# Optimization experiments

Measured on AMD Instinct MI355X. Metric: run time of the kernel, lower is better.

Reference implementation:

```python
import jax, jax.numpy as jnp
import numpy as np

UNITS, LATENT = 512, 128
CMD = max(int(0.4 * (UNITS - LATENT)), 1)   # 153 command neurons (AutoNCP rule)
INTER = (UNITS - LATENT) - CMD              # 231 inter neurons
SIZES = [INTER, CMD, LATENT]                # hidden size of each wiring layer
INS = [1, INTER, CMD]                       # input size of each wiring layer
B, T = 512, 512
SPARSITY = 0.5                              # AutoNCP default sparsity level


def _linear_init(key, out_dim, in_dim):
    k1, k2 = jax.random.split(key)
    lim = 1.0 / np.sqrt(in_dim)
    W = jax.random.uniform(k1, (out_dim, in_dim), minval=-lim, maxval=lim, dtype=jnp.float32)
    b = jax.random.uniform(k2, (out_dim,), minval=-lim, maxval=lim, dtype=jnp.float32)
    return W, b


def setup_inputs() -> dict:
    key = jax.random.key(0)
    ks = jax.random.split(key, 20)
    inp = {
        'elapsed_times': jax.random.uniform(ks[0], (B, T, 1), dtype=jnp.float32),
        'encoder_hidden': jax.random.normal(ks[1], (B, UNITS), dtype=jnp.float32),
    }
    ki = 2
    for l in range(3):
        cat = INS[l] + SIZES[l]
        for name in ('ff1', 'ff2', 'ta', 'tb'):
            W, bvec = _linear_init(ks[ki], SIZES[l], cat); ki += 1
            inp[f'W_{name}_{l}'] = W
            inp[f'b_{name}_{l}'] = bvec
        m = jax.random.bernoulli(ks[ki], 1.0 - SPARSITY, (INS[l], SIZES[l])).astype(jnp.float32); ki += 1
        # WiredCfCCell: recurrent block of the sparsity mask is all-ones; mask is [h, in+h]
        inp[f'mask_{l}'] = jnp.concatenate([m, jnp.ones((SIZES[l], SIZES[l]), jnp.float32)], axis=0).T
    return inp


def _cfc_cell(x_in, h, W1, b1, W2, b2, Wa, ba, Wb, bb, mask):
    x = jnp.concatenate([x_in, h], axis=-1)          # [B, in+h]
    ff1 = jnp.tanh(x @ (W1 * mask).T + b1)
    ff2 = jnp.tanh(x @ (W2 * mask).T + b2)
    # ts = 1.0 (CfC default when no timespans tensor is passed)
    t_interp = jax.nn.sigmoid((x @ Wa.T + ba) + (x @ Wb.T + bb))
    return ff1 * (1.0 - t_interp) + t_interp * ff2


def _forward(elapsed_times, encoder_hidden, layers):
    h0 = encoder_hidden[:, :INTER]
    h1 = encoder_hidden[:, INTER:INTER + CMD]
    h2 = encoder_hidden[:, INTER + CMD:]

    def step(carry, x_t):
        c0, c1, c2 = carry
        n0 = _cfc_cell(x_t, c0, *layers[0])
        n1 = _cfc_cell(n0, c1, *layers[1])
        n2 = _cfc_cell(n1, c2, *layers[2])
        return (n0, n1, n2), n2

    xs = jnp.swapaxes(elapsed_times, 0, 1)           # [T, B, 1]
    (h0, h1, h2), outs = jax.lax.scan(step, (h0, h1, h2), xs)
    rnn_out = jnp.swapaxes(outs, 0, 1)               # [B, T, LATENT]
    rnn_hidden = jnp.concatenate([h0, h1, h2], axis=1)  # [B, UNITS]
    return rnn_out, rnn_hidden


def reference(elapsed_times, encoder_hidden,
              W_ff1_0, b_ff1_0, W_ff2_0, b_ff2_0, W_ta_0, b_ta_0, W_tb_0, b_tb_0, mask_0,
              W_ff1_1, b_ff1_1, W_ff2_1, b_ff2_1, W_ta_1, b_ta_1, W_tb_1, b_tb_1, mask_1,
              W_ff1_2, b_ff1_2, W_ff2_2, b_ff2_2, W_ta_2, b_ta_2, W_tb_2, b_tb_2, mask_2):
    layers = [
        (W_ff1_0, b_ff1_0, W_ff2_0, b_ff2_0, W_ta_0, b_ta_0, W_tb_0, b_tb_0, mask_0),
        (W_ff1_1, b_ff1_1, W_ff2_1, b_ff2_1, W_ta_1, b_ta_1, W_tb_1, b_tb_1, mask_1),
        (W_ff1_2, b_ff1_2, W_ff2_2, b_ff2_2, W_ta_2, b_ta_2, W_tb_2, b_tb_2, mask_2),
    ]
    return _forward(elapsed_times, encoder_hidden, layers)
```

## Files before the change

### kernel.cpp

```cpp
#include <hip/hip_runtime.h>
#include <stdint.h>

#define B_ 512
#define T_ 512

typedef __attribute__((ext_vector_type(8))) __bf16 bf16x8;
typedef __attribute__((ext_vector_type(4))) float f32x4;
typedef __attribute__((ext_vector_type(8))) unsigned short u16x8;

#define N0OFF 1916928u
#define N1OFF 3194880u
#define N2OFF 4046848u
#define FLOFF 4767744u

constexpr int L_[9]   = {0,0,0, 1,1,1,1, 2,2};
constexpr int NT0_[9] = {0,5,10, 0,3,6,8, 0,4};
constexpr int NT_[9]  = {5,5,5, 3,3,2,2, 4,4};
constexpr int KT_[3]  = {8,12,9};
constexpr int NPT_[3] = {15,10,8};
constexpr int SC_[3]  = {231,153,128};
constexpr int RS_[3]  = {264,392,296};
constexpr int CB_[3]  = {0,231,384};
constexpr unsigned WOFF_[3] = {0u,184320u,368640u};
constexpr int RGO_[9] = {0,27,54, 0,16,32,43, 0,22};
constexpr int RGC_[9] = {27,27,24, 16,16,11,9, 22,22};
constexpr int RGV_[9] = {80,80,71, 48,48,32,25, 64,64};
constexpr int RGB_[9] = {0,80,160, 0,48,96,128, 0,64};
constexpr int RCH4_[3] = {312,208,176};
constexpr int WN_[9] = {6,6,6, 5,5,5,5, 1,1};
constexpr int WF_[9][6] = {
  {1,2,3,4,5,6},{0,2,3,4,5,6},{0,1,3,4,5,6},
  {4,5,6,7,8,0},{3,5,6,7,8,0},{3,4,6,7,8,0},{3,4,5,7,8,0},
  {8,0,0,0,0,0},{7,0,0,0,0,0}};
constexpr int WL_[9][6] = {
  {-1,-1,-2,-2,-2,-2},{-1,-1,-2,-2,-2,-2},{-1,-1,-2,-2,-2,-2},
  {-1,-1,-1,-2,-2,0},{-1,-1,-1,-2,-2,0},{-1,-1,-1,-2,-2,0},{-1,-1,-1,-2,-2,0},
  {-1,0,0,0,0,0},{-1,0,0,0,0,0}};

static __device__ __forceinline__ uint16_t bfbits(float f){
  __bf16 h = (__bf16)f; return __builtin_bit_cast(uint16_t, h);
}
static __device__ __forceinline__ float sigm_f(float x){
  return __builtin_amdgcn_rcpf(1.0f + __builtin_amdgcn_exp2f(-1.4426950408889634f*x));
}
static __device__ __forceinline__ float tanh_f(float x){
  return 2.0f*__builtin_amdgcn_rcpf(1.0f + __builtin_amdgcn_exp2f(-2.8853900817779268f*x)) - 1.0f;
}
static __device__ __forceinline__ uint64_t ldg64(const uint16_t* p){
  return __hip_atomic_load((const unsigned long long*)p, __ATOMIC_RELAXED,
                           __HIP_MEMORY_SCOPE_AGENT);
}
static __device__ __forceinline__ void stg64(uint16_t* p, uint64_t v){
  __hip_atomic_store((unsigned long long*)p, v, __ATOMIC_RELAXED,
                     __HIP_MEMORY_SCOPE_AGENT);
}
#define BAR() do { asm volatile("s_waitcnt lgkmcnt(0)" ::: "memory"); \
                   __builtin_amdgcn_s_barrier(); } while(0)
#define DRAIN() asm volatile("s_waitcnt vmcnt(0)" ::: "memory")

__global__ void zero_flags(uint8_t* wsb){
  int i = blockIdx.x*512 + threadIdx.x;
  if (i < 2304) ((int*)(wsb + FLOFF))[i] = 0;
}

__global__ void pack_w(const float* __restrict__ W1, const float* __restrict__ W2,
                       const float* __restrict__ Wa, const float* __restrict__ Wb,
                       const float* __restrict__ Msk, uint16_t* __restrict__ dst,
                       int NPT, int KT, int S, int C)
{
  int c = blockIdx.x * 256 + threadIdx.x;
  int chunks = 3 * NPT * KT * 64;
  if (c >= chunks) return;
  int perN = KT * 64;
  int n3 = c / perN, r = c % perN;
  int kt = r >> 6, lane = r & 63;
  int m = n3 / NPT, nt = n3 % NPT;
  int j = nt * 16 + (lane & 15);
  int kb = kt * 32 + (lane >> 4) * 8;
  u16x8 o;
  #pragma unroll
  for (int i = 0; i < 8; ++i){
    int k = kb + i;
    float v = 0.f;
    if (j < S && k < C){
      size_t idx = (size_t)j * C + k;
      if (m == 0)      v = W1[idx] * Msk[idx];
      else if (m == 1) v = W2[idx] * Msk[idx];
      else             v = Wa[idx] + Wb[idx];
    }
    o[i] = bfbits(v);
  }
  *(u16x8*)(dst + (size_t)c * 8) = o;
}

template<int SID>
__device__ __forceinline__ void stage_run(
    int g, int tid,
    const float* __restrict__ elapsed, const float* __restrict__ enc,
    const float* __restrict__ bp1, const float* __restrict__ bp2,
    const float* __restrict__ bpa, const float* __restrict__ bpb,
    const uint16_t* __restrict__ Wp, uint8_t* __restrict__ wsb,
    float* __restrict__ out, uint16_t* Wl, uint16_t* XA, uint16_t* HST)
{
  constexpr int LAYER = L_[SID];
  constexpr int NT0 = NT0_[SID], NT = NT_[SID];
  constexpr int KT = KT_[LAYER], NPT = NPT_[LAYER];
  constexpr int SCOL = SC_[LAYER], RS = RS_[LAYER];
  constexpr int CBASE = CB_[LAYER];
  constexpr int NCH = RGC_[SID], RGO = RGO_[SID], RGV = RGV_[SID], RGB = RGB_[SID];
  constexpr int RCH4 = RCH4_[LAYER];

  const int wave = tid >> 6, lane = tid & 63, llo = lane & 15, lhi = lane >> 4;
  const int rowg = tid >> 4, cg = tid & 15;
  const int b0 = g * 32;

  uint16_t* R0 = (uint16_t*)(wsb + N0OFF) + (size_t)g * 39936;
  uint16_t* R1 = (uint16_t*)(wsb + N1OFF) + (size_t)g * 26624;
  uint16_t* R2 = (uint16_t*)(wsb + N2OFF) + (size_t)g * 22528;
  int* FLG = (int*)(wsb + FLOFF) + g * (9*16);
  uint16_t* RNG = (LAYER==0) ? R0 : (LAYER==1) ? R1 : R2;

  {
    const u16x8* Wp8 = (const u16x8*)(Wp + WOFF_[LAYER]);
    u16x8* Wl8 = (u16x8*)Wl;
    constexpr int CHUNKS = 3 * NT * KT * 64;
    for (int c = tid; c < CHUNKS; c += 512){
      int m = c / (NT*KT*64), r = c - m*(NT*KT*64);
      int tl = r / (KT*64),  r2 = r - tl*(KT*64);
      Wl8[c] = Wp8[(size_t)((m*NPT + NT0 + tl)*KT*64) + r2];
    }
  }
  for (int i = tid; i < 32*RS; i += 512) XA[i] = 0;

  float bs0 = 0.f, bs1 = 0.f, bs2 = 0.f;
  if (wave < NT){
    const int j = (NT0 + wave)*16 + llo;
    if (j < SCOL){ bs0 = bp1[j]; bs1 = bp2[j]; bs2 = bpa[j] + bpb[j]; }
  }

  auto chunk_store = [&](int slot, uint16_t tag){
    for (int idx = tid; idx < 32*NCH; idx += 512){
      int row = idx / NCH, c = idx - row*NCH;
      int lc = 3*c;
      uint16_t p0 = (lc+0 < RGV) ? HST[row*80 + lc+0] : (uint16_t)0;
      uint16_t p1 = (lc+1 < RGV) ? HST[row*80 + lc+1] : (uint16_t)0;
      uint16_t p2 = (lc+2 < RGV) ? HST[row*80 + lc+2] : (uint16_t)0;
      uint64_t v = (uint64_t)p0 | ((uint64_t)p1<<16) | ((uint64_t)p2<<32)
                 | ((uint64_t)tag<<48);
      stg64(RNG + (size_t)(slot*32 + row)*RCH4 + (size_t)(RGO + c)*4, v);
    }
  };

  for (int idx = tid; idx < 32*NT*16; idx += 512){
    int row = idx / (NT*16), lc = idx % (NT*16);
    int j = RGB + lc;
    float v = (j < SCOL) ? enc[(size_t)(b0+row)*512 + CBASE + j] : 0.f;
    HST[row*80 + lc] = bfbits(v);
  }
  __syncthreads();
  chunk_store(3, 0xFFFFu);
  DRAIN();
  __syncthreads();
  if (tid == 0)
    __hip_atomic_store(&FLG[SID*16], 1, __ATOMIC_RELAXED, __HIP_MEMORY_SCOPE_AGENT);

  const size_t OH = (size_t)B_ * T_ * 128;

  int fc[6];
  #pragma unroll
  for (int i = 0; i < 6; ++i) fc[i] = 1;

  #pragma unroll 1
  for (int t = 0; t < T_; ++t){
    if (tid == 0){
      bool need = false;
      #pragma unroll
      for (int i = 0; i < WN_[SID]; ++i) need |= (fc[i] < t + WL_[SID][i]);
      if (need){
        int spin = 0;
        for (;;){
          bool ok = true;
          #pragma unroll
          for (int i = 0; i < WN_[SID]; ++i){
            if (fc[i] < t + WL_[SID][i])
              fc[i] = __hip_atomic_load(&FLG[WF_[SID][i]*16], __ATOMIC_RELAXED,
                                        __HIP_MEMORY_SCOPE_AGENT);
            ok &= (fc[i] >= t + WL_[SID][i]);
          }
          if (ok) break;
          __builtin_amdgcn_s_sleep(1);
          if ((++spin & 63) == 0)
            (void)__hip_atomic_load(&FLG[WF_[SID][0]*16], __ATOMIC_ACQUIRE,
                                    __HIP_MEMORY_SCOPE_AGENT);
        }
      }
    }
    BAR();

    {
      uint16_t* drow = XA + rowg * RS;
      constexpr int DST0 = (LAYER==0) ? 1 : (LAYER==1) ? 231 : 153;
      for (int lc = cg; lc < RGV; lc += 16)
        drow[DST0 + RGB + lc] = HST[rowg*80 + lc];

      const uint16_t eN = (uint16_t)t, eH = (uint16_t)(t-1);
      if constexpr (LAYER == 0){
        const uint16_t* rb = R0 + (size_t)((((t+3)&3)*32) + rowg) * 312;
        constexpr int OLO = RGO, OHI = RGO + NCH;
        uint64_t v[5]; uint32_t pend = 0;
        #pragma unroll
        for (int i = 0; i < 5; ++i){
          int c = cg + 16*i;
          if (c < 78 && !(c >= OLO && c < OHI)) pend |= 1u<<i;
        }
        while (pend){
          #pragma unroll
          for (int i = 0; i < 5; ++i)
            if (pend & (1u<<i)) v[i] = ldg64(rb + 4*(cg + 16*i));
          uint32_t np = 0;
          #pragma unroll
          for (int i = 0; i < 5; ++i)
            if ((pend & (1u<<i)) && (uint16_t)(v[i]>>48) != eH) np |= 1u<<i;
          pend = np;
          if (pend) __builtin_amdgcn_s_sleep(1);
        }
        #pragma unroll
        for (int i = 0; i < 5; ++i){
          int c = cg + 16*i;
          if (c >= 78 || (c >= OLO && c < OHI)) continue;
          int rgb, rgv, cr;
          if (c < 27){ rgb=0; rgv=80; cr=c; }
          else if (c < 54){ rgb=80; rgv=80; cr=c-27; }
          else { rgb=160; rgv=71; cr=c-54; }
          int base = 3*cr;
          if (base+0 < rgv) drow[1 + rgb + base+0] = (uint16_t)(v[i]);
          if (base+1 < rgv) drow[1 + rgb + base+1] = (uint16_t)(v[i]>>16);
          if (base+2 < rgv) drow[1 + rgb + base+2] = (uint16_t)(v[i]>>32);
        }
        if (cg == 0) drow[0] = bfbits(elapsed[(size_t)(b0 + rowg)*T_ + t]);
      } else if constexpr (LAYER == 1){
        const uint16_t* rbA = R0 + (size_t)(((t&3)*32) + rowg) * 312;
        const uint16_t* rbB = R1 + (size_t)((((t+3)&3)*32) + rowg) * 208;
        constexpr int OLO = RGO, OHI = RGO + NCH;
        uint64_t vA[5], vB[4]; uint32_t pend = 0;
        #pragma unroll
        for (int i = 0; i < 5; ++i){ int c = cg + 16*i; if (c < 78) pend |= 1u<<i; }
        #pragma unroll
        for (int i = 0; i < 4; ++i){
          int c = cg + 16*i;
          if (c < 52 && !(c >= OLO && c < OHI)) pend |= 1u<<(8+i);
        }
        while (pend){
          #pragma unroll
          for (int i = 0; i < 5; ++i)
            if (pend & (1u<<i)) vA[i] = ldg64(rbA + 4*(cg + 16*i));
          #pragma unroll
          for (int i = 0; i < 4; ++i)
            if (pend & (1u<<(8+i))) vB[i] = ldg64(rbB + 4*(cg + 16*i));
          uint32_t np = 0;
          #pragma unroll
          for (int i = 0; i < 5; ++i)
            if ((pend & (1u<<i)) && (uint16_t)(vA[i]>>48) != eN) np |= 1u<<i;
          #pragma unroll
          for (int i = 0; i < 4; ++i)
            if ((pend & (1u<<(8+i))) && (uint16_t)(vB[i]>>48) != eH) np |= 1u<<(8+i);
          pend = np;
          if (pend) __builtin_amdgcn_s_sleep(1);
        }
        #pragma unroll
        for (int i = 0; i < 5; ++i){
          int c = cg + 16*i; if (c >= 78) continue;
          int rgb, rgv, cr;
          if (c < 27){ rgb=0; rgv=80; cr=c; }
          else if (c < 54){ rgb=80; rgv=80; cr=c-27; }
          else { rgb=160; rgv=71; cr=c-54; }
          int base = 3*cr;
          if (base+0 < rgv) drow[rgb + base+0] = (uint16_t)(vA[i]);
          if (base+1 < rgv) drow[rgb + base+1] = (uint16_t)(vA[i]>>16);
          if (base+2 < rgv) drow[rgb + base+2] = (uint16_t)(vA[i]>>32);
        }
        #pragma unroll
        for (int i = 0; i < 4; ++i){
          int c = cg + 16*i;
          if (c >= 52 || (c >= OLO && c < OHI)) continue;
          int rgb, rgv, cr;
          if (c < 16){ rgb=0; rgv=48; cr=c; }
          else if (c < 32){ rgb=48; rgv=48; cr=c-16; }
          else if (c < 43){ rgb=96; rgv=32; cr=c-32; }
          else { rgb=128; rgv=25; cr=c-43; }
          int base = 3*cr;
          if (base+0 < rgv) drow[231 + rgb + base+0] = (uint16_t)(vB[i]);
          if (base+1 < rgv) drow[231 + rgb + base+1] = (uint16_t)(vB[i]>>16);
          if (base+2 < rgv) drow[231 + rgb + base+2] = (uint16_t)(vB[i]>>32);
        }
      } else {
        const uint16_t* rbA = R1 + (size_t)(((t&3)*32) + rowg) * 208;
        const uint16_t* rbB = R2 + (size_t)((((t+3)&3)*32) + rowg) * 176;
        constexpr int OLO = RGO, OHI = RGO + NCH;
        uint64_t vA[4], vB[3]; uint32_t pend = 0;
        #pragma unroll
        for (int i = 0; i < 4; ++i){ int c = cg + 16*i; if (c < 52) pend |= 1u<<i; }
        #pragma unroll
        for (int i = 0; i < 3; ++i){
          int c = cg + 16*i;
          if (c < 44 && !(c >= OLO && c < OHI)) pend |= 1u<<(8+i);
        }
        while (pend){
          #pragma unroll
          for (int i = 0; i < 4; ++i)
            if (pend & (1u<<i)) vA[i] = ldg64(rbA + 4*(cg + 16*i));
          #pragma unroll
          for (int i = 0; i < 3; ++i)
            if (pend & (1u<<(8+i))) vB[i] = ldg64(rbB + 4*(cg + 16*i));
          uint32_t np = 0;
          #pragma unroll
          for (int i = 0; i < 4; ++i)
            if ((pend & (1u<<i)) && (uint16_t)(vA[i]>>48) != eN) np |= 1u<<i;
          #pragma unroll
          for (int i = 0; i < 3; ++i)
            if ((pend & (1u<<(8+i))) && (uint16_t)(vB[i]>>48) != eH) np |= 1u<<(8+i);
          pend = np;
          if (pend) __builtin_amdgcn_s_sleep(1);
        }
        #pragma unroll
        for (int i = 0; i < 4; ++i){
          int c = cg + 16*i; if (c >= 52) continue;
          int rgb, rgv, cr;
          if (c < 16){ rgb=0; rgv=48; cr=c; }
          else if (c < 32){ rgb=48; rgv=48; cr=c-16; }
          else if (c < 43){ rgb=96; rgv=32; cr=c-32; }
          else { rgb=128; rgv=25; cr=c-43; }
          int base = 3*cr;
          if (base+0 < rgv) drow[rgb + base+0] = (uint16_t)(vA[i]);
          if (base+1 < rgv) drow[rgb + base+1] = (uint16_t)(vA[i]>>16);
          if (base+2 < rgv) drow[rgb + base+2] = (uint16_t)(vA[i]>>32);
        }
        #pragma unroll
        for (int i = 0; i < 3; ++i){
          int c = cg + 16*i;
          if (c >= 44 || (c >= OLO && c < OHI)) continue;
          int rgb, cr;
          if (c < 22){ rgb=0; cr=c; } else { rgb=64; cr=c-22; }
          int base = 3*cr;
          if (base+0 < 64) drow[153 + rgb + base+0] = (uint16_t)(vB[i]);
          if (base+1 < 64) drow[153 + rgb + base+1] = (uint16_t)(vB[i]>>16);
          if (base+2 < 64) drow[153 + rgb + base+2] = (uint16_t)(vB[i]>>32);
        }
      }
    }
    BAR();
    if (tid == 0)
      __hip_atomic_store(&FLG[SID*16], t+2, __ATOMIC_RELAXED, __HIP_MEMORY_SCOPE_AGENT);

    float hsave[8];
    if (wave < NT){
      bf16x8 aL[KT], aH[KT];
      const uint16_t* ar = XA + llo*RS + lhi*8;
      #pragma unroll
      for (int kt = 0; kt < KT; ++kt){
        aL[kt] = *(const bf16x8*)(ar + kt*32);
        aH[kt] = *(const bf16x8*)(ar + 16*RS + kt*32);
      }
      f32x4 cL0 = {0.f,0.f,0.f,0.f}, cL1 = cL0, cL2 = cL0;
      f32x4 cH0 = cL0, cH1 = cL0, cH2 = cL0;
      #pragma unroll
      for (int m = 0; m < 3; ++m){
        const uint16_t* wb = Wl + (size_t)((m*NT + wave)*KT)*512 + lane*8;
        #pragma unroll
        for (int kt = 0; kt < KT; ++kt){
          bf16x8 w = *(const bf16x8*)(wb + kt*512);
          if (m == 0){ cL0 = __builtin_amdgcn_mfma_f32_16x16x32_bf16(aL[kt], w, cL0,0,0,0);
                       cH0 = __builtin_amdgcn_mfma_f32_16x16x32_bf16(aH[kt], w, cH0,0,0,0); }
          else if (m == 1){ cL1 = __builtin_amdgcn_mfma_f32_16x16x32_bf16(aL[kt], w, cL1,0,0,0);
                            cH1 = __builtin_amdgcn_mfma_f32_16x16x32_bf16(aH[kt], w, cH1,0,0,0); }
          else { cL2 = __builtin_amdgcn_mfma_f32_16x16x32_bf16(aL[kt], w, cL2,0,0,0);
                 cH2 = __builtin_amdgcn_mfma_f32_16x16x32_bf16(aH[kt], w, cH2,0,0,0); }
        }
      }
      #pragma unroll
      for (int half = 0; half < 2; ++half){
        const f32x4& c0 = half ? cH0 : cL0;
        const f32x4& c1 = half ? cH1 : cL1;
        const f32x4& c2 = half ? cH2 : cL2;
        #pragma unroll
        for (int r = 0; r < 4; ++r){
          const int row = half*16 + lhi*4 + r;
          float ff1 = tanh_f(c0[r] + bs0);
          float ff2 = tanh_f(c1[r] + bs1);
          float tt  = sigm_f(c2[r] + bs2);
          float h = ff1 + tt*(ff2 - ff1);
          HST[row*80 + wave*16 + llo] = bfbits(h);
          hsave[half*4 + r] = h;
        }
      }
    }
    BAR();

    chunk_store(t & 3, (uint16_t)t);

    if (wave < NT){
      const int j = (NT0 + wave)*16 + llo;
      if constexpr (LAYER == 2){
        #pragma unroll
        for (int half = 0; half < 2; ++half)
          #pragma unroll
          for (int r = 0; r < 4; ++r){
            const int row = half*16 + lhi*4 + r;
            out[((size_t)(b0+row)*T_ + t)*128 + j] = hsave[half*4 + r];
          }
      }
      if (t == T_-1 && j < SCOL){
        #pragma unroll
        for (int half = 0; half < 2; ++half)
          #pragma unroll
          for (int r = 0; r < 4; ++r){
            const int row = half*16 + lhi*4 + r;
            out[OH + (size_t)(b0+row)*512 + CBASE + j] = hsave[half*4 + r];
          }
      }
    }
  }
}

__global__ __launch_bounds__(512) void cfc_pipe(
    const float* __restrict__ elapsed, const float* __restrict__ enc,
    const float* __restrict__ b1_0, const float* __restrict__ b2_0,
    const float* __restrict__ ba0,  const float* __restrict__ bb0,
    const float* __restrict__ b1_1, const float* __restrict__ b2_1,
    const float* __restrict__ ba1,  const float* __restrict__ bb1,
    const float* __restrict__ b1_2, const float* __restrict__ b2_2,
    const float* __restrict__ ba2,  const float* __restrict__ bb2,
    const uint16_t* __restrict__ Wp, uint8_t* __restrict__ wsb,
    float* __restrict__ out)
{
  __shared__ uint16_t Wl[61440];
  __shared__ uint16_t XA[12544];
  __shared__ uint16_t HST[2560];

  const int bid = blockIdx.x;
  const int g = bid & 15, s = bid >> 4;
  const int tid = threadIdx.x;

  switch (s){
    case 0: stage_run<0>(g, tid, elapsed, enc, b1_0, b2_0, ba0, bb0, Wp, wsb, out, Wl, XA, HST); break;
    case 1: stage_run<1>(g, tid, elapsed, enc, b1_0, b2_0, ba0, bb0, Wp, wsb, out, Wl, XA, HST); break;
    case 2: stage_run<2>(g, tid, elapsed, enc, b1_0, b2_0, ba0, bb0, Wp, wsb, out, Wl, XA, HST); break;
    case 3: stage_run<3>(g, tid, elapsed, enc, b1_1, b2_1, ba1, bb1, Wp, wsb, out, Wl, XA, HST); break;
    case 4: stage_run<4>(g, tid, elapsed, enc, b1_1, b2_1, ba1, bb1, Wp, wsb, out, Wl, XA, HST); break;
    case 5: stage_run<5>(g, tid, elapsed, enc, b1_1, b2_1, ba1, bb1, Wp, wsb, out, Wl, XA, HST); break;
    case 6: stage_run<6>(g, tid, elapsed, enc, b1_1, b2_1, ba1, bb1, Wp, wsb, out, Wl, XA, HST); break;
    case 7: stage_run<7>(g, tid, elapsed, enc, b1_2, b2_2, ba2, bb2, Wp, wsb, out, Wl, XA, HST); break;
    default: stage_run<8>(g, tid, elapsed, enc, b1_2, b2_2, ba2, bb2, Wp, wsb, out, Wl, XA, HST); break;
  }
}

extern "C" void kernel_launch(void* const* d_in, const int* in_sizes, int n_in,
                              void* d_out, int out_size, void* d_ws, size_t ws_size,
                              hipStream_t stream)
{
  const float* elapsed = (const float*)d_in[0];
  const float* enc     = (const float*)d_in[1];
  const float* W1_0 = (const float*)d_in[2];  const float* b1_0 = (const float*)d_in[3];
  const float* W2_0 = (const float*)d_in[4];  const float* b2_0 = (const float*)d_in[5];
  const float* Wa0  = (const float*)d_in[6];  const float* ba0  = (const float*)d_in[7];
  const float* Wb0  = (const float*)d_in[8];  const float* bb0  = (const float*)d_in[9];
  const float* M0   = (const float*)d_in[10];
  const float* W1_1 = (const float*)d_in[11]; const float* b1_1 = (const float*)d_in[12];
  const float* W2_1 = (const float*)d_in[13]; const float* b2_1 = (const float*)d_in[14];
  const float* Wa1  = (const float*)d_in[15]; const float* ba1  = (const float*)d_in[16];
  const float* Wb1  = (const float*)d_in[17]; const float* bb1  = (const float*)d_in[18];
  const float* M1   = (const float*)d_in[19];
  const float* W1_2 = (const float*)d_in[20]; const float* b1_2 = (const float*)d_in[21];
  const float* W2_2 = (const float*)d_in[22]; const float* b2_2 = (const float*)d_in[23];
  const float* Wa2  = (const float*)d_in[24]; const float* ba2  = (const float*)d_in[25];
  const float* Wb2  = (const float*)d_in[26]; const float* bb2  = (const float*)d_in[27];
  const float* M2   = (const float*)d_in[28];

  uint8_t*  wsb = (uint8_t*)d_ws;
  uint16_t* wp  = (uint16_t*)d_ws;

  zero_flags<<<5, 512, 0, stream>>>(wsb);
  pack_w<<<90, 256, 0, stream>>>(W1_0, W2_0, Wa0, Wb0, M0, wp,          15,  8, 231, 232);
  pack_w<<<90, 256, 0, stream>>>(W1_1, W2_1, Wa1, Wb1, M1, wp + 184320, 10, 12, 153, 384);
  pack_w<<<54, 256, 0, stream>>>(W1_2, W2_2, Wa2, Wb2, M2, wp + 368640,  8,  9, 128, 281);

  cfc_pipe<<<144, 512, 0, stream>>>(elapsed, enc,
                                    b1_0, b2_0, ba0, bb0,
                                    b1_1, b2_1, ba1, bb1,
                                    b1_2, b2_2, ba2, bb2,
                                    wp, wsb, (float*)d_out);
}
```

Before: 2.434 ms.

## Have each pipeline block serve two batch groups alternately, halving the grid

Each persistent stage block now handles two batch groups (g and g+8) and interleaves their timestep phases, so the grid shrinks from 144 to 72 blocks. Each block keeps one copy of its weight slice in LDS and reuses it for both groups, and while one group waits on its upstream flags the other group's work can proceed. The cost is that each block does twice the serial work per timestep. It also needs a second HST buffer in shared memory.

```diff
diff --git a/kernel.cpp b/kernel.cpp
--- a/kernel.cpp
+++ b/kernel.cpp
@@ -95,12 +95,13 @@
 
 template<int SID>
 __device__ __forceinline__ void stage_run(
-    int g, int tid,
+    int gA, int gB, int tid,
     const float* __restrict__ elapsed, const float* __restrict__ enc,
     const float* __restrict__ bp1, const float* __restrict__ bp2,
     const float* __restrict__ bpa, const float* __restrict__ bpb,
     const uint16_t* __restrict__ Wp, uint8_t* __restrict__ wsb,
-    float* __restrict__ out, uint16_t* Wl, uint16_t* XA, uint16_t* HST)
+    float* __restrict__ out, uint16_t* Wl, uint16_t* XA,
+    uint16_t* HSTA, uint16_t* HSTB)
 {
   constexpr int LAYER = L_[SID];
   constexpr int NT0 = NT0_[SID], NT = NT_[SID];
@@ -112,13 +113,18 @@
 
   const int wave = tid >> 6, lane = tid & 63, llo = lane & 15, lhi = lane >> 4;
   const int rowg = tid >> 4, cg = tid & 15;
-  const int b0 = g * 32;
-
-  uint16_t* R0 = (uint16_t*)(wsb + N0OFF) + (size_t)g * 39936;
-  uint16_t* R1 = (uint16_t*)(wsb + N1OFF) + (size_t)g * 26624;
-  uint16_t* R2 = (uint16_t*)(wsb + N2OFF) + (size_t)g * 22528;
-  int* FLG = (int*)(wsb + FLOFF) + g * (9*16);
-  uint16_t* RNG = (LAYER==0) ? R0 : (LAYER==1) ? R1 : R2;
+  const size_t OH = (size_t)B_ * T_ * 128;
+
+  uint16_t* R0A = (uint16_t*)(wsb + N0OFF) + (size_t)gA * 39936;
+  uint16_t* R1A = (uint16_t*)(wsb + N1OFF) + (size_t)gA * 26624;
+  uint16_t* R2A = (uint16_t*)(wsb + N2OFF) + (size_t)gA * 22528;
+  uint16_t* R0B = (uint16_t*)(wsb + N0OFF) + (size_t)gB * 39936;
+  uint16_t* R1B = (uint16_t*)(wsb + N1OFF) + (size_t)gB * 26624;
+  uint16_t* R2B = (uint16_t*)(wsb + N2OFF) + (size_t)gB * 22528;
+  int* FLGA = (int*)(wsb + FLOFF) + gA * (9*16);
+  int* FLGB = (int*)(wsb + FLOFF) + gB * (9*16);
+  uint16_t* RNGA = (LAYER==0) ? R0A : (LAYER==1) ? R1A : R2A;
+  uint16_t* RNGB = (LAYER==0) ? R0B : (LAYER==1) ? R1B : R2B;
 
   {
     const u16x8* Wp8 = (const u16x8*)(Wp + WOFF_[LAYER]);
@@ -138,40 +144,46 @@
     if (j < SCOL){ bs0 = bp1[j]; bs1 = bp2[j]; bs2 = bpa[j] + bpb[j]; }
   }
 
-  auto chunk_store = [&](int slot, uint16_t tag){
+  auto chunk_store = [&](uint16_t* RNGg, uint16_t* HSTg, int slot, uint16_t tag){
     for (int idx = tid; idx < 32*NCH; idx += 512){
       int row = idx / NCH, c = idx - row*NCH;
       int lc = 3*c;
-      uint16_t p0 = (lc+0 < RGV) ? HST[row*80 + lc+0] : (uint16_t)0;
-      uint16_t p1 = (lc+1 < RGV) ? HST[row*80 + lc+1] : (uint16_t)0;
-      uint16_t p2 = (lc+2 < RGV) ? HST[row*80 + lc+2] : (uint16_t)0;
+      uint16_t p0 = (lc+0 < RGV) ? HSTg[row*80 + lc+0] : (uint16_t)0;
+      uint16_t p1 = (lc+1 < RGV) ? HSTg[row*80 + lc+1] : (uint16_t)0;
+      uint16_t p2 = (lc+2 < RGV) ? HSTg[row*80 + lc+2] : (uint16_t)0;
       uint64_t v = (uint64_t)p0 | ((uint64_t)p1<<16) | ((uint64_t)p2<<32)
                  | ((uint64_t)tag<<48);
-      stg64(RNG + (size_t)(slot*32 + row)*RCH4 + (size_t)(RGO + c)*4, v);
+      stg64(RNGg + (size_t)(slot*32 + row)*RCH4 + (size_t)(RGO + c)*4, v);
     }
   };
 
-  for (int idx = tid; idx < 32*NT*16; idx += 512){
-    int row = idx / (NT*16), lc = idx % (NT*16);
-    int j = RGB + lc;
-    float v = (j < SCOL) ? enc[(size_t)(b0+row)*512 + CBASE + j] : 0.f;
-    HST[row*80 + lc] = bfbits(v);
+  #pragma unroll
+  for (int gi = 0; gi < 2; ++gi){
+    const int b0 = (gi ? gB : gA) * 32;
+    uint16_t* HSTg = gi ? HSTB : HSTA;
+    for (int idx = tid; idx < 32*NT*16; idx += 512){
+      int row = idx / (NT*16), lc = idx % (NT*16);
+      int j = RGB + lc;
+      float v = (j < SCOL) ? enc[(size_t)(b0+row)*512 + CBASE + j] : 0.f;
+      HSTg[row*80 + lc] = bfbits(v);
+    }
   }
   __syncthreads();
-  chunk_store(3, 0xFFFFu);
+  chunk_store(RNGA, HSTA, 3, 0xFFFFu);
+  chunk_store(RNGB, HSTB, 3, 0xFFFFu);
   DRAIN();
   __syncthreads();
-  if (tid == 0)
-    __hip_atomic_store(&FLG[SID*16], 1, __ATOMIC_RELAXED, __HIP_MEMORY_SCOPE_AGENT);
-
-  const size_t OH = (size_t)B_ * T_ * 128;
-
-  int fc[6];
+  if (tid == 0){
+    __hip_atomic_store(&FLGA[SID*16], 1, __ATOMIC_RELAXED, __HIP_MEMORY_SCOPE_AGENT);
+    __hip_atomic_store(&FLGB[SID*16], 1, __ATOMIC_RELAXED, __HIP_MEMORY_SCOPE_AGENT);
+  }
+
+  int fcA[6], fcB[6];
   #pragma unroll
-  for (int i = 0; i < 6; ++i) fc[i] = 1;
-
-  #pragma unroll 1
-  for (int t = 0; t < T_; ++t){
+  for (int i = 0; i < 6; ++i){ fcA[i] = 1; fcB[i] = 1; }
+
+  auto do_phase = [&](int* FLG, uint16_t* R0g, uint16_t* R1g, uint16_t* R2g,
+                      uint16_t* RNGg, uint16_t* HSTg, int b0, int (&fc)[6], int t){
     if (tid == 0){
       bool need = false;
       #pragma unroll
@@ -201,11 +213,11 @@
       uint16_t* drow = XA + rowg * RS;
       constexpr int DST0 = (LAYER==0) ? 1 : (LAYER==1) ? 231 : 153;
       for (int lc = cg; lc < RGV; lc += 16)
-        drow[DST0 + RGB + lc] = HST[rowg*80 + lc];
+        drow[DST0 + RGB + lc] = HSTg[rowg*80 + lc];
 
       const uint16_t eN = (uint16_t)t, eH = (uint16_t)(t-1);
       if constexpr (LAYER == 0){
-        const uint16_t* rb = R0 + (size_t)((((t+3)&3)*32) + rowg) * 312;
+        const uint16_t* rb = R0g + (size_t)((((t+3)&3)*32) + rowg) * 312;
         constexpr int OLO = RGO, OHI = RGO + NCH;
         uint64_t v[5]; uint32_t pend = 0;
         #pragma unroll
@@ -239,8 +251,8 @@
         }
         if (cg == 0) drow[0] = bfbits(elapsed[(size_t)(b0 + rowg)*T_ + t]);
       } else if constexpr (LAYER == 1){
-        const uint16_t* rbA = R0 + (size_t)(((t&3)*32) + rowg) * 312;
-        const uint16_t* rbB = R1 + (size_t)((((t+3)&3)*32) + rowg) * 208;
+        const uint16_t* rbA = R0g + (size_t)(((t&3)*32) + rowg) * 312;
+        const uint16_t* rbB = R1g + (size_t)((((t+3)&3)*32) + rowg) * 208;
         constexpr int OLO = RGO, OHI = RGO + NCH;
         uint64_t vA[5], vB[4]; uint32_t pend = 0;
         #pragma unroll
@@ -294,8 +306,8 @@
           if (base+2 < rgv) drow[231 + rgb + base+2] = (uint16_t)(vB[i]>>32);
         }
       } else {
-        const uint16_t* rbA = R1 + (size_t)(((t&3)*32) + rowg) * 208;
-        const uint16_t* rbB = R2 + (size_t)((((t+3)&3)*32) + rowg) * 176;
+        const uint16_t* rbA = R1g + (size_t)(((t&3)*32) + rowg) * 208;
+        const uint16_t* rbB = R2g + (size_t)((((t+3)&3)*32) + rowg) * 176;
         constexpr int OLO = RGO, OHI = RGO + NCH;
         uint64_t vA[4], vB[3]; uint32_t pend = 0;
         #pragma unroll
@@ -389,14 +401,14 @@
           float ff2 = tanh_f(c1[r] + bs1);
           float tt  = sigm_f(c2[r] + bs2);
           float h = ff1 + tt*(ff2 - ff1);
-          HST[row*80 + wave*16 + llo] = bfbits(h);
+          HSTg[row*80 + wave*16 + llo] = bfbits(h);
           hsave[half*4 + r] = h;
         }
       }
     }
     BAR();
 
-    chunk_store(t & 3, (uint16_t)t);
+    chunk_store(RNGg, HSTg, t & 3, (uint16_t)t);
 
     if (wave < NT){
       const int j = (NT0 + wave)*16 + llo;
@@ -419,6 +431,12 @@
           }
       }
     }
+  };
+
+  #pragma unroll 1
+  for (int t = 0; t < T_; ++t){
+    do_phase(FLGA, R0A, R1A, R2A, RNGA, HSTA, gA*32, fcA, t);
+    do_phase(FLGB, R0B, R1B, R2B, RNGB, HSTB, gB*32, fcB, t);
   }
 }
 
@@ -435,22 +453,25 @@
 {
   __shared__ uint16_t Wl[61440];
   __shared__ uint16_t XA[12544];
-  __shared__ uint16_t HST[2560];
+  __shared__ uint16_t HST[5120];
 
   const int bid = blockIdx.x;
-  const int g = bid & 15, s = bid >> 4;
+  const int p = bid & 7, s = bid >> 3;
+  const int gA = p, gB = p + 8;
   const int tid = threadIdx.x;
+  uint16_t* HSTA = HST;
+  uint16_t* HSTB = HST + 2560;
 
   switch (s){
-    case 0: stage_run<0>(g, tid, elapsed, enc, b1_0, b2_0, ba0, bb0, Wp, wsb, out, Wl, XA, HST); break;
-    case 1: stage_run<1>(g, tid, elapsed, enc, b1_0, b2_0, ba0, bb0, Wp, wsb, out, Wl, XA, HST); break;
-    case 2: stage_run<2>(g, tid, elapsed, enc, b1_0, b2_0, ba0, bb0, Wp, wsb, out, Wl, XA, HST); break;
-    case 3: stage_run<3>(g, tid, elapsed, enc, b1_1, b2_1, ba1, bb1, Wp, wsb, out, Wl, XA, HST); break;
-    case 4: stage_run<4>(g, tid, elapsed, enc, b1_1, b2_1, ba1, bb1, Wp, wsb, out, Wl, XA, HST); break;
-    case 5: stage_run<5>(g, tid, elapsed, enc, b1_1, b2_1, ba1, bb1, Wp, wsb, out, Wl, XA, HST); break;
-    case 6: stage_run<6>(g, tid, elapsed, enc, b1_1, b2_1, ba1, bb1, Wp, wsb, out, Wl, XA, HST); break;
-    case 7: stage_run<7>(g, tid, elapsed, enc, b1_2, b2_2, ba2, bb2, Wp, wsb, out, Wl, XA, HST); break;
-    default: stage_run<8>(g, tid, elapsed, enc, b1_2, b2_2, ba2, bb2, Wp, wsb, out, Wl, XA, HST); break;
+    case 0: stage_run<0>(gA, gB, tid, elapsed, enc, b1_0, b2_0, ba0, bb0, Wp, wsb, out, Wl, XA, HSTA, HSTB); break;
+    case 1: stage_run<1>(gA, gB, tid, elapsed, enc, b1_0, b2_0, ba0, bb0, Wp, wsb, out, Wl, XA, HSTA, HSTB); break;
+    case 2: stage_run<2>(gA, gB, tid, elapsed, enc, b1_0, b2_0, ba0, bb0, Wp, wsb, out, Wl, XA, HSTA, HSTB); break;
+    case 3: stage_run<3>(gA, gB, tid, elapsed, enc, b1_1, b2_1, ba1, bb1, Wp, wsb, out, Wl, XA, HSTA, HSTB); break;
+    case 4: stage_run<4>(gA, gB, tid, elapsed, enc, b1_1, b2_1, ba1, bb1, Wp, wsb, out, Wl, XA, HSTA, HSTB); break;
+    case 5: stage_run<5>(gA, gB, tid, elapsed, enc, b1_1, b2_1, ba1, bb1, Wp, wsb, out, Wl, XA, HSTA, HSTB); break;
+    case 6: stage_run<6>(gA, gB, tid, elapsed, enc, b1_1, b2_1, ba1, bb1, Wp, wsb, out, Wl, XA, HSTA, HSTB); break;
+    case 7: stage_run<7>(gA, gB, tid, elapsed, enc, b1_2, b2_2, ba2, bb2, Wp, wsb, out, Wl, XA, HSTA, HSTB); break;
+    default: stage_run<8>(gA, gB, tid, elapsed, enc, b1_2, b2_2, ba2, bb2, Wp, wsb, out, Wl, XA, HSTA, HSTB); break;
   }
 }
 
@@ -484,9 +505,9 @@
   pack_w<<<90, 256, 0, stream>>>(W1_1, W2_1, Wa1, Wb1, M1, wp + 184320, 10, 12, 153, 384);
   pack_w<<<54, 256, 0, stream>>>(W1_2, W2_2, Wa2, Wb2, M2, wp + 368640,  8,  9, 128, 281);
 
-  cfc_pipe<<<144, 512, 0, stream>>>(elapsed, enc,
-                                    b1_0, b2_0, ba0, bb0,
-                                    b1_1, b2_1, ba1, bb1,
-                                    b1_2, b2_2, ba2, bb2,
-                                    wp, wsb, (float*)d_out);
-}
+  cfc_pipe<<<72, 512, 0, stream>>>(elapsed, enc,
+                                   b1_0, b2_0, ba0, bb0,
+                                   b1_1, b2_1, ba1, bb1,
+                                   b1_2, b2_2, ba2, bb2,
+                                   wp, wsb, (float*)d_out);
+}
```

Result: slower. 4.867 ms (+99.9%).
